# Optimization experiments

Measured on AMD Instinct MI355X. Metric: run time of the kernel, lower is better.

## Reference

```python
import jax, jax.numpy as jnp
import numpy as np

B, S, D, H, L, W, O = 4, 1024, 512, 8, 6, 64, 300
DH = D // H          # head dim = 64
R = 2 * W + 3        # rel_proj output dim = 131
EPS = 1e-6


def setup_inputs() -> dict:
    key = jax.random.key(0)
    ks = jax.random.split(key, 12)
    sc = 0.02
    x = jax.random.normal(ks[0], (B, S, D), jnp.float32)
    inp = {
        "x": x,
        "ln1_g": jnp.ones((L, D), jnp.float32),
        "ln1_b": jnp.zeros((L, D), jnp.float32),
        "qkv_w": jax.random.normal(ks[1], (L, D, 3 * D), jnp.float32) * sc,
        "qkv_b": jnp.zeros((L, 3 * D), jnp.float32),
        "rel_w": jax.random.normal(ks[2], (DH, R), jnp.float32) * sc,
        "rel_b": jnp.zeros((R,), jnp.float32),
        "ln2_g": jnp.ones((L, D), jnp.float32),
        "ln2_b": jnp.zeros((L, D), jnp.float32),
        "mlp_w1": jax.random.normal(ks[3], (L, D, 4 * D), jnp.float32) * sc,
        "mlp_b1": jnp.zeros((L, 4 * D), jnp.float32),
        "mlp_w2": jax.random.normal(ks[4], (L, 4 * D, D), jnp.float32) * sc,
        "mlp_b2": jnp.zeros((L, D), jnp.float32),
        "normf_g": jnp.ones((D,), jnp.float32),
        "normf_b": jnp.zeros((D,), jnp.float32),
        "head_w": jax.random.normal(ks[5], (D, O), jnp.float32) * sc,
        "head_b": jnp.zeros((O,), jnp.float32),
        "mask": jax.random.randint(ks[6], (B, O), 0, 2, jnp.int32),
    }
    return inp


def _layernorm(x, g, b):
    m = jnp.mean(x, axis=-1, keepdims=True)
    v = jnp.mean(jnp.square(x - m), axis=-1, keepdims=True)
    return (x - m) * jax.lax.rsqrt(v + EPS) * g + b


def _forward(x, ln1_g, ln1_b, qkv_w, qkv_b, rel_w, rel_b, ln2_g, ln2_b,
             mlp_w1, mlp_b1, mlp_w2, mlp_b2, normf_g, normf_b, head_w, head_b, mask):
    b, s, d = x.shape
    # clamped relative offsets, shifted to [0, 2W]; shape [s, s]
    ar = jnp.arange(s)
    offsets = jnp.clip(ar[None, :] - ar[:, None], -W, W) + W
    off_bh = jnp.broadcast_to(offsets[None, None], (b, H, s, s))
    scale = 1.0 / np.sqrt(D / H)  # = 1/sqrt(dh)

    def block(xc, lp):
        (l1g, l1b, qw, qb, l2g, l2b, w1, b1, w2, b2) = lp
        h = _layernorm(xc, l1g, l1b)
        qkv = (h @ qw + qb).reshape(b, s, H, 3 * DH)
        q, k, v = jnp.split(qkv, 3, axis=-1)            # [b,s,h,dh] each
        q = q.transpose(0, 2, 1, 3)                     # [b,h,s,dh]
        k = k.transpose(0, 2, 1, 3)
        v = v.transpose(0, 2, 1, 3)
        content = jnp.einsum('bhik,bhjk->bhij', q, k) * scale
        pos = q @ rel_w + rel_b                          # [b,h,s,R]
        pos_scores = jnp.take_along_axis(pos, off_bh, axis=-1)  # [b,h,s,s]
        attn = jax.nn.softmax(content + pos_scores, axis=-1)
        out = jnp.einsum('bhij,bhjk->bhik', attn, v)     # [b,h,s,dh]
        xc = xc + out.transpose(0, 2, 1, 3).reshape(b, s, d)
        h2 = _layernorm(xc, l2g, l2b)
        m = jax.nn.gelu(h2 @ w1 + b1, approximate=False) @ w2 + b2
        return xc + m, None

    layer_params = (ln1_g, ln1_b, qkv_w, qkv_b, ln2_g, ln2_b,
                    mlp_w1, mlp_b1, mlp_w2, mlp_b2)
    x, _ = jax.lax.scan(block, x, layer_params)
    x = _layernorm(x, normf_g, normf_b)[:, 0, :]         # CLS token
    logits = x @ head_w + head_b                          # [b, O]
    return jnp.where(mask == 0, -jnp.inf, logits)


def reference(x, ln1_g, ln1_b, qkv_w, qkv_b, rel_w, rel_b, ln2_g, ln2_b,
              mlp_w1, mlp_b1, mlp_w2, mlp_b2, normf_g, normf_b, head_w, head_b, mask):
    return _forward(x, ln1_g, ln1_b, qkv_w, qkv_b, rel_w, rel_b, ln2_g, ln2_b,
                    mlp_w1, mlp_b1, mlp_w2, mlp_b2, normf_g, normf_b, head_w, head_b, mask)
```

## Files before the change

### kernel.cpp

```cpp
#include <hip/hip_runtime.h>
#include <math.h>

#define B_  4
#define S_  1024
#define D_  512
#define H_  8
#define L_  6
#define W_  64
#define O_  300
#define DH_ 64
#define R_  131
#define R2_ 132

typedef __attribute__((ext_vector_type(8))) short bf16x8;
typedef __attribute__((ext_vector_type(4))) float f32x4;

#define SWZ(r) ((((r) ^ ((r) >> 3)) & 7) << 4)

__device__ __forceinline__ float gelu_f(float x) {
    return 0.5f * x * (1.0f + erff(x * 0.70710678118654752f));
}

__device__ __forceinline__ unsigned short f2bf(float f) {
    union { float f; unsigned u; } c; c.f = f;
    unsigned u = c.u;
    unsigned r = (u + 0x7fffu + ((u >> 16) & 1u)) >> 16;
    return (unsigned short)r;
}
__device__ __forceinline__ float bf2f(unsigned short u) {
    union { unsigned u; float f; } c; c.u = ((unsigned)u) << 16; return c.f;
}

__device__ __forceinline__ void gload_lds16(const void* g, void* l) {
    __builtin_amdgcn_global_load_lds(
        (const __attribute__((address_space(1))) unsigned int*)g,
        (__attribute__((address_space(3))) unsigned int*)l, 16, 0, 0);
}

template<int OB>
__global__ __launch_bounds__(256) void ln_kernel(
    const float* __restrict__ x, const float* __restrict__ g,
    const float* __restrict__ b, void* __restrict__ y,
    int rows, long instride, long outstride)
{
    int wave = threadIdx.x >> 6;
    int lane = threadIdx.x & 63;
    int row  = blockIdx.x * 4 + wave;
    if (row >= rows) return;
    const float* xr = x + (size_t)row * instride;
    float4 v0 = *(const float4*)(xr + lane * 4);
    float4 v1 = *(const float4*)(xr + 256 + lane * 4);

    float s = v0.x + v0.y + v0.z + v0.w + v1.x + v1.y + v1.z + v1.w;
    #pragma unroll
    for (int off = 32; off >= 1; off >>= 1) s += __shfl_xor(s, off);
    float mean = s * (1.0f / 512.0f);

    float a0 = v0.x - mean, a1 = v0.y - mean, a2 = v0.z - mean, a3 = v0.w - mean;
    float a4 = v1.x - mean, a5 = v1.y - mean, a6 = v1.z - mean, a7 = v1.w - mean;
    float vs = a0*a0 + a1*a1 + a2*a2 + a3*a3 + a4*a4 + a5*a5 + a6*a6 + a7*a7;
    #pragma unroll
    for (int off = 32; off >= 1; off >>= 1) vs += __shfl_xor(vs, off);
    float rstd = rsqrtf(vs * (1.0f / 512.0f) + 1e-6f);

    float4 g0 = *(const float4*)(g + lane * 4);
    float4 g1 = *(const float4*)(g + 256 + lane * 4);
    float4 b0 = *(const float4*)(b + lane * 4);
    float4 b1 = *(const float4*)(b + 256 + lane * 4);

    float o0 = a0 * rstd * g0.x + b0.x;
    float o1 = a1 * rstd * g0.y + b0.y;
    float o2 = a2 * rstd * g0.z + b0.z;
    float o3 = a3 * rstd * g0.w + b0.w;
    float o4 = a4 * rstd * g1.x + b1.x;
    float o5 = a5 * rstd * g1.y + b1.y;
    float o6 = a6 * rstd * g1.z + b1.z;
    float o7 = a7 * rstd * g1.w + b1.w;

    if (OB) {
        unsigned short* yr = (unsigned short*)y + (size_t)row * outstride;
        ushort4 p0 = {f2bf(o0), f2bf(o1), f2bf(o2), f2bf(o3)};
        ushort4 p1 = {f2bf(o4), f2bf(o5), f2bf(o6), f2bf(o7)};
        *(ushort4*)(yr + lane * 4)       = p0;
        *(ushort4*)(yr + 256 + lane * 4) = p1;
    } else {
        float* yr = (float*)y + (size_t)row * outstride;
        *(float4*)(yr + lane * 4)       = make_float4(o0, o1, o2, o3);
        *(float4*)(yr + 256 + lane * 4) = make_float4(o4, o5, o6, o7);
    }
}

__global__ __launch_bounds__(256) void tconv_kernel(
    const float* __restrict__ in, unsigned short* __restrict__ out, int K, int N)
{
    __shared__ float t[32][33];
    int tx = threadIdx.x & 31, ty = threadIdx.x >> 5;
    int n0 = blockIdx.x * 32, k0 = blockIdx.y * 32;
    #pragma unroll
    for (int j = 0; j < 4; ++j)
        t[ty + 8*j][tx] = in[(size_t)(k0 + ty + 8*j) * N + n0 + tx];
    __syncthreads();
    #pragma unroll
    for (int j = 0; j < 4; ++j)
        out[(size_t)(n0 + ty + 8*j) * K + k0 + tx] = f2bf(t[tx][ty + 8*j]);
}

__global__ __launch_bounds__(256) void relw_prep(
    const float* __restrict__ rel_w, unsigned short* __restrict__ relwT)
{
    for (int i = threadIdx.x; i < 144 * 64; i += 256) {
        int r = i >> 6, c = i & 63;
        relwT[i] = (r < R_) ? f2bf(rel_w[(size_t)c * R_ + r]) : (unsigned short)0;
    }
}

template<int ACT, int OBF, int BM, int BN, int WM, int WN, int BK>
__global__ __launch_bounds__(256) void mfma_gemm(
    const unsigned short* __restrict__ A, const unsigned short* __restrict__ BT,
    const float* __restrict__ bias, const float* __restrict__ resid,
    void* __restrict__ Cout, int M, int N, int K)
{
    static_assert(WM * WN == 4, "4 waves");
    constexpr int MFR = BM / WM / 16;
    constexpr int NFR = BN / WN / 16;
    constexpr int TPR = BK / 8;
    constexpr int RPP = 256 / TPR;
    __shared__ __align__(16) unsigned short As[BM * BK];
    __shared__ __align__(16) unsigned short Bs[BN * BK];
    int tid  = threadIdx.x;
    int lane = tid & 63;
    int l15 = lane & 15, l4 = lane >> 4;
    int wid  = tid >> 6;
    int wave_m = (wid / WN) * (BM / WM);
    int wave_n = (wid % WN) * (BN / WN);
    int bm = blockIdx.y * BM, bn = blockIdx.x * BN;

    const f32x4 z4 = {0.f, 0.f, 0.f, 0.f};
    f32x4 acc[MFR][NFR];
    #pragma unroll
    for (int m = 0; m < MFR; ++m)
        #pragma unroll
        for (int n = 0; n < NFR; ++n) acc[m][n] = z4;

    int arow = tid / TPR;
    int acol8 = ((tid % TPR) ^ (arow & (TPR - 1))) * 8;
    const unsigned short* Ab = A  + (size_t)(bm + arow) * K + acol8;
    const unsigned short* Bb = BT + (size_t)(bn + arow) * K + acol8;
    unsigned short* Adst = As + tid * 8;
    unsigned short* Bdst = Bs + tid * 8;

    int swzA = l15 & (TPR - 1);
    const unsigned short* Afrag = As + (size_t)(wave_m + l15) * BK;
    const unsigned short* Bfrag = Bs + (size_t)(wave_n + l15) * BK;

    for (int k0 = 0; k0 < K; k0 += BK) {
        #pragma unroll
        for (int ch = 0; ch < BM / RPP; ++ch)
            gload_lds16(Ab + (size_t)ch * RPP * K + k0, Adst + ch * RPP * BK);
        #pragma unroll
        for (int ch = 0; ch < BN / RPP; ++ch)
            gload_lds16(Bb + (size_t)ch * RPP * K + k0, Bdst + ch * RPP * BK);
        __syncthreads();

        #pragma unroll
        for (int kk = 0; kk < BK / 32; ++kk) {
            int off8 = ((l4 + 4 * kk) ^ swzA) * 8;
            bf16x8 af[MFR], bfr[NFR];
            #pragma unroll
            for (int m = 0; m < MFR; ++m) af[m]  = *(const bf16x8*)(Afrag + m * 16 * BK + off8);
            #pragma unroll
            for (int n = 0; n < NFR; ++n) bfr[n] = *(const bf16x8*)(Bfrag + n * 16 * BK + off8);
            #pragma unroll
            for (int m = 0; m < MFR; ++m)
                #pragma unroll
                for (int n = 0; n < NFR; ++n)
                    acc[m][n] = __builtin_amdgcn_mfma_f32_16x16x32_bf16(af[m], bfr[n], acc[m][n], 0, 0, 0);
        }
        __syncthreads();
    }

    int r0 = bm + wave_m + (l4 * 4);
    int c0 = bn + wave_n + l15;
    #pragma unroll
    for (int m = 0; m < MFR; ++m) {
        #pragma unroll
        for (int n = 0; n < NFR; ++n) {
            int c = c0 + n * 16;
            float bv = bias[c];
            #pragma unroll
            for (int q = 0; q < 4; ++q) {
                int r = r0 + m * 16 + q;
                float v = acc[m][n][q] + bv;
                if (ACT == 1) v = gelu_f(v);
                if (resid) v += resid[(size_t)r * N + c];
                if (OBF) ((unsigned short*)Cout)[(size_t)r * N + c] = f2bf(v);
                else     ((float*)Cout)[(size_t)r * N + c] = v;
            }
        }
    }
}

__global__ __launch_bounds__(512, 2) void attn_mfma(
    const unsigned short* __restrict__ qkv,
    const unsigned short* __restrict__ relwT,
    const float* __restrict__ rel_b,
    float* __restrict__ xres)
{
    __shared__ __align__(16) unsigned char shm[66048];
    unsigned char* Klds  = shm;
    unsigned char* Vtlds = shm + 16384;
    unsigned char* Plds  = shm + 32768;
    unsigned short* pos16 = (unsigned short*)(shm + 49152);
    float* mergeO  = (float*)shm;
    float* mergeML = (float*)(shm + 17408);

    int tid = threadIdx.x, lane = tid & 63, w = tid >> 6;
    int l15 = lane & 15, l4 = lane >> 4;
    int wq = w & 3;
    int g  = w >> 2;
    int it0 = blockIdx.x * 64;
    int h = blockIdx.y, b = blockIdx.z;
    const float LOG2E = 1.4426950408889634f;
    const float SC = 0.125f * LOG2E;

    bf16x8 qa[2];
    {
        const unsigned short* qp = qkv + (size_t)(b * S_ + it0 + wq * 16 + l15) * 1536 + h * 192 + l4 * 8;
        qa[0] = *(const bf16x8*)(qp);
        qa[1] = *(const bf16x8*)(qp + 32);
    }

    if (g == 0) {
        #pragma unroll
        for (int n = 0; n < 9; ++n) {
            f32x4 pacc = {0.f, 0.f, 0.f, 0.f};
            #pragma unroll
            for (int ks = 0; ks < 2; ++ks) {
                bf16x8 bv = *(const bf16x8*)(relwT + (size_t)(16 * n + l15) * 64 + ks * 32 + l4 * 8);
                pacc = __builtin_amdgcn_mfma_f32_16x16x32_bf16(qa[ks], bv, pacc, 0, 0, 0);
            }
            int c = 16 * n + l15;
            if (c < R_) {
                float rb = rel_b[c];
                #pragma unroll
                for (int q = 0; q < 4; ++q)
                    pos16[(wq * 16 + l4 * 4 + q) * R2_ + c] = f2bf((pacc[q] + rb) * LOG2E);
            }
        }
    }
    __syncthreads();

    int rloc = wq * 16 + l15;
    int i_glob = it0 + rloc;
    float p_lo = bf2f(pos16[rloc * R2_ + 0]);
    float p_hi = bf2f(pos16[rloc * R2_ + 128]);

    int rf = tid >> 2, seg = tid & 3;
    int gk = rf >> 6, rr = rf & 63;
    const unsigned short* kbase = qkv + (size_t)(b * S_ + gk * 512 + rr) * 1536 + h * 192 + 64 + seg * 16;
    int kbyt = gk * 8192 + ((rr * 128 + seg * 32) ^ SWZ(rr));
    int pf = tid >> 3, seg8 = tid & 7;
    int gv = pf >> 5, pp = pf & 31;
    const unsigned short* vbase = qkv + (size_t)(b * S_ + gv * 512 + 2 * pp) * 1536 + h * 192 + 128 + seg8 * 8;
    bf16x8 kr0, kr1, vr0, vr1;
    kr0 = *(const bf16x8*)(kbase);
    kr1 = *(const bf16x8*)(kbase + 8);
    vr0 = *(const bf16x8*)(vbase);
    vr1 = *(const bf16x8*)(vbase + 1536);

    const f32x4 z4 = {0.f, 0.f, 0.f, 0.f};
    f32x4 oacc[4];
    #pragma unroll
    for (int n = 0; n < 4; ++n) oacc[n] = z4;
    float mrun_s = -INFINITY, lrun_s = 0.f;
    int wmin = it0 + wq * 16;
    unsigned char* Kw = Klds + g * 8192;
    unsigned char* Vw = Vtlds + g * 8192;
    unsigned char* Pw = Plds + w * 2048;

    for (int t = 0; t < 8; ++t) {
        int jt0 = g * 512 + t * 64;
        __syncthreads();
        *(bf16x8*)(Klds + kbyt) = kr0;
        *(bf16x8*)(Klds + (kbyt ^ 16)) = kr1;
        #pragma unroll
        for (int i = 0; i < 8; ++i) {
            int dh = seg8 * 8 + i;
            unsigned v01 = (unsigned)(unsigned short)vr0[i] | ((unsigned)(unsigned short)vr1[i] << 16);
            *(unsigned*)(Vtlds + gv * 8192 + ((dh * 128 + pp * 4) ^ SWZ(dh))) = v01;
        }
        __syncthreads();
        if (t < 7) {
            const unsigned short* kp = kbase + (size_t)(t + 1) * 64 * 1536;
            kr0 = *(const bf16x8*)(kp);
            kr1 = *(const bf16x8*)(kp + 8);
            const unsigned short* vp = vbase + (size_t)(t + 1) * 64 * 1536;
            vr0 = *(const bf16x8*)(vp);
            vr1 = *(const bf16x8*)(vp + 1536);
        }

        f32x4 ssw[4];
        #pragma unroll
        for (int n = 0; n < 4; ++n) ssw[n] = z4;
        #pragma unroll
        for (int n = 0; n < 4; ++n) {
            int kvr = 16 * n + l15;
            #pragma unroll
            for (int ks = 0; ks < 2; ++ks) {
                bf16x8 ak = *(const bf16x8*)(Kw + ((kvr * 128 + ks * 64 + l4 * 16) ^ SWZ(kvr)));
                ssw[n] = __builtin_amdgcn_mfma_f32_16x16x32_bf16(ak, qa[ks], ssw[n], 0, 0, 0);
            }
        }

        float sv[4][4];
        bool left  = (jt0 + 63 < wmin - 64);
        bool right = (jt0 > wmin + 15 + 64);
        if (left || right) {
            float pc = left ? p_lo : p_hi;
            #pragma unroll
            for (int n = 0; n < 4; ++n)
                #pragma unroll
                for (int r = 0; r < 4; ++r) sv[n][r] = fmaf(ssw[n][r], SC, pc);
        } else {
            #pragma unroll
            for (int n = 0; n < 4; ++n)
                #pragma unroll
                for (int r = 0; r < 4; ++r) {
                    int j = jt0 + 16 * n + l4 * 4 + r;
                    int off = j - i_glob;
                    off = off < -64 ? -64 : (off > 64 ? 64 : off);
                    sv[n][r] = fmaf(ssw[n][r], SC, bf2f(pos16[rloc * R2_ + off + 64]));
                }
        }

        float a0 = fmaxf(fmaxf(sv[0][0], sv[0][1]), fmaxf(sv[0][2], sv[0][3]));
        float a1 = fmaxf(fmaxf(sv[1][0], sv[1][1]), fmaxf(sv[1][2], sv[1][3]));
        float a2 = fmaxf(fmaxf(sv[2][0], sv[2][1]), fmaxf(sv[2][2], sv[2][3]));
        float a3 = fmaxf(fmaxf(sv[3][0], sv[3][1]), fmaxf(sv[3][2], sv[3][3]));
        float mx = fmaxf(fmaxf(a0, a1), fmaxf(a2, a3));
        mx = fmaxf(mx, __shfl_xor(mx, 16));
        mx = fmaxf(mx, __shfl_xor(mx, 32));
        float mnew = fmaxf(mrun_s, mx);
        float al = exp2f(mrun_s - mnew);
        mrun_s = mnew;
        float rs = 0.f;
        #pragma unroll
        for (int n = 0; n < 4; ++n)
            #pragma unroll
            for (int r = 0; r < 4; ++r) {
                float p = exp2f(sv[n][r] - mnew);
                sv[n][r] = p;
                rs += p;
            }
        rs += __shfl_xor(rs, 16);
        rs += __shfl_xor(rs, 32);
        lrun_s = lrun_s * al + rs;
        float alv0 = __shfl(al, l4 * 4 + 0);
        float alv1 = __shfl(al, l4 * 4 + 1);
        float alv2 = __shfl(al, l4 * 4 + 2);
        float alv3 = __shfl(al, l4 * 4 + 3);
        #pragma unroll
        for (int n = 0; n < 4; ++n) {
            oacc[n][0] *= alv0; oacc[n][1] *= alv1;
            oacc[n][2] *= alv2; oacc[n][3] *= alv3;
        }

        #pragma unroll
        for (int n = 0; n < 4; ++n) {
            unsigned pk01, pk23;
            asm("v_cvt_pk_bf16_f32 %0, %1, %2" : "=v"(pk01) : "v"(sv[n][0]), "v"(sv[n][1]));
            asm("v_cvt_pk_bf16_f32 %0, %1, %2" : "=v"(pk23) : "v"(sv[n][2]), "v"(sv[n][3]));
            int boff = (l15 * 128 + (16 * n + l4 * 4) * 2) ^ SWZ(l15);
            *(uint2*)(Pw + boff) = make_uint2(pk01, pk23);
        }

        bf16x8 pa[2];
        #pragma unroll
        for (int ks = 0; ks < 2; ++ks)
            pa[ks] = *(const bf16x8*)(Pw + ((l15 * 128 + ks * 64 + l4 * 16) ^ SWZ(l15)));
        #pragma unroll
        for (int n = 0; n < 4; ++n) {
            int dh = 16 * n + l15;
            #pragma unroll
            for (int ks = 0; ks < 2; ++ks) {
                bf16x8 bv = *(const bf16x8*)(Vw + ((dh * 128 + ks * 64 + l4 * 16) ^ SWZ(dh)));
                oacc[n] = __builtin_amdgcn_mfma_f32_16x16x32_bf16(pa[ks], bv, oacc[n], 0, 0, 0);
            }
        }
    }

    __syncthreads();
    if (g == 1) {
        #pragma unroll
        for (int n = 0; n < 4; ++n)
            #pragma unroll
            for (int r = 0; r < 4; ++r)
                mergeO[(wq * 16 + l4 * 4 + r) * 68 + 16 * n + l15] = oacc[n][r];
        if (lane < 16) {
            mergeML[rloc * 2 + 0] = mrun_s;
            mergeML[rloc * 2 + 1] = lrun_s;
        }
    }
    __syncthreads();
    if (g == 0) {
        float mb = mergeML[rloc * 2 + 0];
        float lb = mergeML[rloc * 2 + 1];
        float M  = fmaxf(mrun_s, mb);
        float fa = exp2f(mrun_s - M);
        float fb = exp2f(mb - M);
        float inv = 1.0f / (lrun_s * fa + lb * fb);
        float A_s = fa * inv, B_s = fb * inv;
        float Av[4], Bv[4];
        #pragma unroll
        for (int r = 0; r < 4; ++r) {
            Av[r] = __shfl(A_s, l4 * 4 + r);
            Bv[r] = __shfl(B_s, l4 * 4 + r);
        }
        #pragma unroll
        for (int r = 0; r < 4; ++r) {
            int row = wq * 16 + l4 * 4 + r;
            float* xp = xres + (size_t)(b * S_ + it0 + row) * D_ + h * DH_;
            #pragma unroll
            for (int n = 0; n < 4; ++n)
                xp[16 * n + l15] += oacc[n][r] * Av[r] + mergeO[row * 68 + 16 * n + l15] * Bv[r];
        }
    }
}

__global__ __launch_bounds__(256) void head_kernel(
    const float* __restrict__ hin, const float* __restrict__ hw,
    const float* __restrict__ hbias, const int* __restrict__ mask,
    float* __restrict__ out)
{
    __shared__ float a[4][512];
    __shared__ float part[4][64][4];
    int tid = threadIdx.x;
    #pragma unroll
    for (int i = tid; i < 2048; i += 256) a[i >> 9][i & 511] = hin[i];
    __syncthreads();

    int cl = tid & 63;
    int c  = blockIdx.x * 64 + cl;
    int ks = tid >> 6;
    float ac[4] = {0.f, 0.f, 0.f, 0.f};
    if (c < O_) {
        const float* wp = hw + (size_t)(ks * 128) * O_ + c;
        #pragma unroll 8
        for (int k = 0; k < 128; ++k) {
            float wv = wp[(size_t)k * O_];
            int kk = ks * 128 + k;
            ac[0] = fmaf(a[0][kk], wv, ac[0]);
            ac[1] = fmaf(a[1][kk], wv, ac[1]);
            ac[2] = fmaf(a[2][kk], wv, ac[2]);
            ac[3] = fmaf(a[3][kk], wv, ac[3]);
        }
    }
    #pragma unroll
    for (int bb = 0; bb < 4; ++bb) part[ks][cl][bb] = ac[bb];
    __syncthreads();
    if (ks == 0 && c < O_) {
        float hbv = hbias[c];
        #pragma unroll
        for (int bb = 0; bb < 4; ++bb) {
            float v = part[0][cl][bb] + part[1][cl][bb] + part[2][cl][bb] + part[3][cl][bb] + hbv;
            out[bb * O_ + c] = (mask[bb * O_ + c] == 0) ? -1e30f : v;
        }
    }
}

extern "C" void kernel_launch(void* const* d_in, const int* in_sizes, int n_in,
                              void* d_out, int out_size, void* d_ws, size_t ws_size,
                              hipStream_t stream) {
    const float* x      = (const float*)d_in[0];
    const float* ln1_g  = (const float*)d_in[1];
    const float* ln1_b  = (const float*)d_in[2];
    const float* qkv_w  = (const float*)d_in[3];
    const float* qkv_b  = (const float*)d_in[4];
    const float* rel_w  = (const float*)d_in[5];
    const float* rel_b  = (const float*)d_in[6];
    const float* ln2_g  = (const float*)d_in[7];
    const float* ln2_b  = (const float*)d_in[8];
    const float* mlp_w1 = (const float*)d_in[9];
    const float* mlp_b1 = (const float*)d_in[10];
    const float* mlp_w2 = (const float*)d_in[11];
    const float* mlp_b2 = (const float*)d_in[12];
    const float* normf_g = (const float*)d_in[13];
    const float* normf_b = (const float*)d_in[14];
    const float* head_w  = (const float*)d_in[15];
    const float* head_b  = (const float*)d_in[16];
    const int*   mask    = (const int*)d_in[17];
    float* out = (float*)d_out;
    float* ws  = (float*)d_ws;

    float* x_cur = ws;
    float* reg2  = ws + 2097152;
    float* wregs = ws + 6291456;
    unsigned short* qkv16 = (unsigned short*)reg2;
    unsigned short* midb  = (unsigned short*)reg2;
    unsigned short* hb    = (unsigned short*)wregs;
    unsigned short* wTq   = (unsigned short*)(wregs + 1048576);
    unsigned short* wT1   = (unsigned short*)(wregs + 1441792);
    unsigned short* wT2   = (unsigned short*)(wregs + 1966080);
    unsigned short* relwT = (unsigned short*)(ws + 10616832);
    float* head_in = ws + 10621440;

    const int NR = B_ * S_;
    dim3 blk(256);

    hipMemcpyAsync(x_cur, x, (size_t)NR * D_ * sizeof(float),
                   hipMemcpyDeviceToDevice, stream);
    relw_prep<<<1, blk, 0, stream>>>(rel_w, relwT);

    for (int l = 0; l < L_; ++l) {
        ln_kernel<1><<<NR / 4, blk, 0, stream>>>(x_cur, ln1_g + l * D_, ln1_b + l * D_,
                                                 hb, NR, D_, D_);
        tconv_kernel<<<dim3(48, 16), blk, 0, stream>>>(
            qkv_w + (size_t)l * D_ * 3 * D_, wTq, D_, 3 * D_);
        mfma_gemm<0, 1, 128, 64, 4, 1, 64><<<dim3(24, 32), blk, 0, stream>>>(
            hb, wTq, qkv_b + (size_t)l * 3 * D_, nullptr, qkv16, NR, 3 * D_, D_);
        attn_mfma<<<dim3(S_ / 64, H_, B_), dim3(512), 0, stream>>>(qkv16, relwT, rel_b, x_cur);
        ln_kernel<1><<<NR / 4, blk, 0, stream>>>(x_cur, ln2_g + l * D_, ln2_b + l * D_,
                                                 hb, NR, D_, D_);
        tconv_kernel<<<dim3(64, 16), blk, 0, stream>>>(
            mlp_w1 + (size_t)l * D_ * 4 * D_, wT1, D_, 4 * D_);
        mfma_gemm<1, 1, 128, 64, 4, 1, 64><<<dim3(32, 32), blk, 0, stream>>>(
            hb, wT1, mlp_b1 + (size_t)l * 4 * D_, nullptr, midb, NR, 4 * D_, D_);
        tconv_kernel<<<dim3(16, 64), blk, 0, stream>>>(
            mlp_w2 + (size_t)l * 4 * D_ * D_, wT2, 4 * D_, D_);
        mfma_gemm<0, 0, 64, 64, 2, 2, 64><<<dim3(8, 64), blk, 0, stream>>>(
            midb, wT2, mlp_b2 + (size_t)l * D_, x_cur, x_cur, NR, D_, 4 * D_);
    }

    ln_kernel<0><<<1, blk, 0, stream>>>(x_cur, normf_g, normf_b, head_in,
                                        B_, (long)S_ * D_, D_);
    head_kernel<<<dim3(5), blk, 0, stream>>>(head_in, head_w, head_b, mask, out);
}
```

Before: 706.0 us.

## Batch weight conversion, swizzle GEMM blocks, lazy softmax rescale, fuse final LN

When the workspace is large enough, all layers' weight transposes and bf16 conversions now run in one up-front kernel, replacing three conversion launches per layer. GEMM workgroup ids are remapped in an XCD-aware way to improve L2 locality. The attention online softmax skips rescaling unless the running max grows past a threshold. The final layernorm is fused into the head kernel. Together these cut launch count and per-tile exp and multiply work, at the cost of a larger workspace and a slight numerical risk from the deferred rescale.

```diff
diff --git a/kernel.cpp b/kernel.cpp
--- a/kernel.cpp
+++ b/kernel.cpp
@@ -37,17 +37,15 @@
         (__attribute__((address_space(3))) unsigned int*)l, 16, 0, 0);
 }
 
-template<int OB>
 __global__ __launch_bounds__(256) void ln_kernel(
     const float* __restrict__ x, const float* __restrict__ g,
-    const float* __restrict__ b, void* __restrict__ y,
-    int rows, long instride, long outstride)
+    const float* __restrict__ b, unsigned short* __restrict__ y, int rows)
 {
     int wave = threadIdx.x >> 6;
     int lane = threadIdx.x & 63;
     int row  = blockIdx.x * 4 + wave;
     if (row >= rows) return;
-    const float* xr = x + (size_t)row * instride;
+    const float* xr = x + (size_t)row * D_;
     float4 v0 = *(const float4*)(xr + lane * 4);
     float4 v1 = *(const float4*)(xr + 256 + lane * 4);
 
@@ -68,26 +66,13 @@
     float4 b0 = *(const float4*)(b + lane * 4);
     float4 b1 = *(const float4*)(b + 256 + lane * 4);
 
-    float o0 = a0 * rstd * g0.x + b0.x;
-    float o1 = a1 * rstd * g0.y + b0.y;
-    float o2 = a2 * rstd * g0.z + b0.z;
-    float o3 = a3 * rstd * g0.w + b0.w;
-    float o4 = a4 * rstd * g1.x + b1.x;
-    float o5 = a5 * rstd * g1.y + b1.y;
-    float o6 = a6 * rstd * g1.z + b1.z;
-    float o7 = a7 * rstd * g1.w + b1.w;
-
-    if (OB) {
-        unsigned short* yr = (unsigned short*)y + (size_t)row * outstride;
-        ushort4 p0 = {f2bf(o0), f2bf(o1), f2bf(o2), f2bf(o3)};
-        ushort4 p1 = {f2bf(o4), f2bf(o5), f2bf(o6), f2bf(o7)};
-        *(ushort4*)(yr + lane * 4)       = p0;
-        *(ushort4*)(yr + 256 + lane * 4) = p1;
-    } else {
-        float* yr = (float*)y + (size_t)row * outstride;
-        *(float4*)(yr + lane * 4)       = make_float4(o0, o1, o2, o3);
-        *(float4*)(yr + 256 + lane * 4) = make_float4(o4, o5, o6, o7);
-    }
+    unsigned short* yr = y + (size_t)row * D_;
+    ushort4 p0 = {f2bf(a0 * rstd * g0.x + b0.x), f2bf(a1 * rstd * g0.y + b0.y),
+                  f2bf(a2 * rstd * g0.z + b0.z), f2bf(a3 * rstd * g0.w + b0.w)};
+    ushort4 p1 = {f2bf(a4 * rstd * g1.x + b1.x), f2bf(a5 * rstd * g1.y + b1.y),
+                  f2bf(a6 * rstd * g1.z + b1.z), f2bf(a7 * rstd * g1.w + b1.w)};
+    *(ushort4*)(yr + lane * 4)       = p0;
+    *(ushort4*)(yr + 256 + lane * 4) = p1;
 }
 
 __global__ __launch_bounds__(256) void tconv_kernel(
@@ -112,6 +97,46 @@
         int r = i >> 6, c = i & 63;
         relwT[i] = (r < R_) ? f2bf(rel_w[(size_t)c * R_ + r]) : (unsigned short)0;
     }
+}
+
+__global__ __launch_bounds__(256) void prep_all(
+    const float* __restrict__ qkv_w, const float* __restrict__ mlp_w1,
+    const float* __restrict__ mlp_w2, const float* __restrict__ rel_w,
+    unsigned short* __restrict__ wTq_all, unsigned short* __restrict__ wT1_all,
+    unsigned short* __restrict__ wT2_all, unsigned short* __restrict__ relwT)
+{
+    int bid = blockIdx.x;
+    if (bid >= 16896) {
+        for (int i = threadIdx.x; i < 144 * 64; i += 256) {
+            int r = i >> 6, c = i & 63;
+            relwT[i] = (r < R_) ? f2bf(rel_w[(size_t)c * R_ + r]) : (unsigned short)0;
+        }
+        return;
+    }
+    int l = bid / 2816, rr = bid - l * 2816;
+    const float* in; unsigned short* out; int K, N, bx, by;
+    if (rr < 768) {
+        in = qkv_w + (size_t)l * 512 * 1536; out = wTq_all + (size_t)l * 1536 * 512;
+        K = 512; N = 1536; bx = rr % 48; by = rr / 48;
+    } else if (rr < 1792) {
+        int r2 = rr - 768;
+        in = mlp_w1 + (size_t)l * 512 * 2048; out = wT1_all + (size_t)l * 2048 * 512;
+        K = 512; N = 2048; bx = r2 % 64; by = r2 / 64;
+    } else {
+        int r2 = rr - 1792;
+        in = mlp_w2 + (size_t)l * 2048 * 512; out = wT2_all + (size_t)l * 512 * 2048;
+        K = 2048; N = 512; bx = r2 % 16; by = r2 / 16;
+    }
+    __shared__ float t[32][33];
+    int tx = threadIdx.x & 31, ty = threadIdx.x >> 5;
+    int n0 = bx * 32, k0 = by * 32;
+    #pragma unroll
+    for (int j = 0; j < 4; ++j)
+        t[ty + 8*j][tx] = in[(size_t)(k0 + ty + 8*j) * N + n0 + tx];
+    __syncthreads();
+    #pragma unroll
+    for (int j = 0; j < 4; ++j)
+        out[(size_t)(n0 + ty + 8*j) * K + k0 + tx] = f2bf(t[tx][ty + 8*j]);
 }
 
 template<int ACT, int OBF, int BM, int BN, int WM, int WN, int BK>
@@ -133,7 +158,11 @@
     int wid  = tid >> 6;
     int wave_m = (wid / WN) * (BM / WM);
     int wave_n = (wid % WN) * (BN / WN);
-    int bm = blockIdx.y * BM, bn = blockIdx.x * BN;
+
+    int nwg = gridDim.x * gridDim.y;
+    int bid0 = blockIdx.y * gridDim.x + blockIdx.x;
+    int bid = (bid0 & 7) * (nwg >> 3) + (bid0 >> 3);
+    int bm = (bid / gridDim.x) * BM, bn = (bid % gridDim.x) * BN;
 
     const f32x4 z4 = {0.f, 0.f, 0.f, 0.f};
     f32x4 acc[MFR][NFR];
@@ -222,6 +251,7 @@
     int h = blockIdx.y, b = blockIdx.z;
     const float LOG2E = 1.4426950408889634f;
     const float SC = 0.125f * LOG2E;
+    const float THR = 11.5441f;
 
     bf16x8 qa[2];
     {
@@ -340,30 +370,33 @@
         float mx = fmaxf(fmaxf(a0, a1), fmaxf(a2, a3));
         mx = fmaxf(mx, __shfl_xor(mx, 16));
         mx = fmaxf(mx, __shfl_xor(mx, 32));
-        float mnew = fmaxf(mrun_s, mx);
-        float al = exp2f(mrun_s - mnew);
-        mrun_s = mnew;
+        if (!__all(mx - mrun_s <= THR)) {
+            float mnew = fmaxf(mrun_s, mx);
+            float al = exp2f(mrun_s - mnew);
+            mrun_s = mnew;
+            lrun_s *= al;
+            float alv0 = __shfl(al, l4 * 4 + 0);
+            float alv1 = __shfl(al, l4 * 4 + 1);
+            float alv2 = __shfl(al, l4 * 4 + 2);
+            float alv3 = __shfl(al, l4 * 4 + 3);
+            #pragma unroll
+            for (int n = 0; n < 4; ++n) {
+                oacc[n][0] *= alv0; oacc[n][1] *= alv1;
+                oacc[n][2] *= alv2; oacc[n][3] *= alv3;
+            }
+        }
         float rs = 0.f;
         #pragma unroll
         for (int n = 0; n < 4; ++n)
             #pragma unroll
             for (int r = 0; r < 4; ++r) {
-                float p = exp2f(sv[n][r] - mnew);
+                float p = exp2f(sv[n][r] - mrun_s);
                 sv[n][r] = p;
                 rs += p;
             }
         rs += __shfl_xor(rs, 16);
         rs += __shfl_xor(rs, 32);
-        lrun_s = lrun_s * al + rs;
-        float alv0 = __shfl(al, l4 * 4 + 0);
-        float alv1 = __shfl(al, l4 * 4 + 1);
-        float alv2 = __shfl(al, l4 * 4 + 2);
-        float alv3 = __shfl(al, l4 * 4 + 3);
-        #pragma unroll
-        for (int n = 0; n < 4; ++n) {
-            oacc[n][0] *= alv0; oacc[n][1] *= alv1;
-            oacc[n][2] *= alv2; oacc[n][3] *= alv3;
-        }
+        lrun_s += rs;
 
         #pragma unroll
         for (int n = 0; n < 4; ++n) {
@@ -428,15 +461,42 @@
 }
 
 __global__ __launch_bounds__(256) void head_kernel(
-    const float* __restrict__ hin, const float* __restrict__ hw,
+    const float* __restrict__ xc, const float* __restrict__ gf,
+    const float* __restrict__ bfp, const float* __restrict__ hw,
     const float* __restrict__ hbias, const int* __restrict__ mask,
     float* __restrict__ out)
 {
     __shared__ float a[4][512];
     __shared__ float part[4][64][4];
     int tid = threadIdx.x;
-    #pragma unroll
-    for (int i = tid; i < 2048; i += 256) a[i >> 9][i & 511] = hin[i];
+    int wv = tid >> 6, lane = tid & 63;
+    {
+        const float* xr = xc + (size_t)wv * S_ * D_;
+        float4 v0 = *(const float4*)(xr + lane * 4);
+        float4 v1 = *(const float4*)(xr + 256 + lane * 4);
+        float s = v0.x + v0.y + v0.z + v0.w + v1.x + v1.y + v1.z + v1.w;
+        #pragma unroll
+        for (int off = 32; off >= 1; off >>= 1) s += __shfl_xor(s, off);
+        float mean = s * (1.0f / 512.0f);
+        float c0 = v0.x - mean, c1 = v0.y - mean, c2 = v0.z - mean, c3 = v0.w - mean;
+        float c4 = v1.x - mean, c5 = v1.y - mean, c6 = v1.z - mean, c7 = v1.w - mean;
+        float vs = c0*c0 + c1*c1 + c2*c2 + c3*c3 + c4*c4 + c5*c5 + c6*c6 + c7*c7;
+        #pragma unroll
+        for (int off = 32; off >= 1; off >>= 1) vs += __shfl_xor(vs, off);
+        float rstd = rsqrtf(vs * (1.0f / 512.0f) + 1e-6f);
+        float4 g0 = *(const float4*)(gf + lane * 4);
+        float4 g1 = *(const float4*)(gf + 256 + lane * 4);
+        float4 b0 = *(const float4*)(bfp + lane * 4);
+        float4 b1 = *(const float4*)(bfp + 256 + lane * 4);
+        a[wv][lane * 4 + 0] = c0 * rstd * g0.x + b0.x;
+        a[wv][lane * 4 + 1] = c1 * rstd * g0.y + b0.y;
+        a[wv][lane * 4 + 2] = c2 * rstd * g0.z + b0.z;
+        a[wv][lane * 4 + 3] = c3 * rstd * g0.w + b0.w;
+        a[wv][256 + lane * 4 + 0] = c4 * rstd * g1.x + b1.x;
+        a[wv][256 + lane * 4 + 1] = c5 * rstd * g1.y + b1.y;
+        a[wv][256 + lane * 4 + 2] = c6 * rstd * g1.z + b1.z;
+        a[wv][256 + lane * 4 + 3] = c7 * rstd * g1.w + b1.w;
+    }
     __syncthreads();
 
     int cl = tid & 63;
@@ -447,12 +507,12 @@
         const float* wp = hw + (size_t)(ks * 128) * O_ + c;
         #pragma unroll 8
         for (int k = 0; k < 128; ++k) {
-            float wv = wp[(size_t)k * O_];
+            float wvv = wp[(size_t)k * O_];
             int kk = ks * 128 + k;
-            ac[0] = fmaf(a[0][kk], wv, ac[0]);
-            ac[1] = fmaf(a[1][kk], wv, ac[1]);
-            ac[2] = fmaf(a[2][kk], wv, ac[2]);
-            ac[3] = fmaf(a[3][kk], wv, ac[3]);
+            ac[0] = fmaf(a[0][kk], wvv, ac[0]);
+            ac[1] = fmaf(a[1][kk], wvv, ac[1]);
+            ac[2] = fmaf(a[2][kk], wvv, ac[2]);
+            ac[3] = fmaf(a[3][kk], wvv, ac[3]);
         }
     }
     #pragma unroll
@@ -492,46 +552,72 @@
     float* out = (float*)d_out;
     float* ws  = (float*)d_ws;
 
+    const int NR = B_ * S_;
+    dim3 blk(256);
+
     float* x_cur = ws;
     float* reg2  = ws + 2097152;
-    float* wregs = ws + 6291456;
     unsigned short* qkv16 = (unsigned short*)reg2;
     unsigned short* midb  = (unsigned short*)reg2;
-    unsigned short* hb    = (unsigned short*)wregs;
-    unsigned short* wTq   = (unsigned short*)(wregs + 1048576);
-    unsigned short* wT1   = (unsigned short*)(wregs + 1441792);
-    unsigned short* wT2   = (unsigned short*)(wregs + 1966080);
-    unsigned short* relwT = (unsigned short*)(ws + 10616832);
-    float* head_in = ws + 10621440;
-
-    const int NR = B_ * S_;
-    dim3 blk(256);
 
     hipMemcpyAsync(x_cur, x, (size_t)NR * D_ * sizeof(float),
                    hipMemcpyDeviceToDevice, stream);
-    relw_prep<<<1, blk, 0, stream>>>(rel_w, relwT);
-
-    for (int l = 0; l < L_; ++l) {
-        ln_kernel<1><<<NR / 4, blk, 0, stream>>>(x_cur, ln1_g + l * D_, ln1_b + l * D_,
-                                                 hb, NR, D_, D_);
-        tconv_kernel<<<dim3(48, 16), blk, 0, stream>>>(
-            qkv_w + (size_t)l * D_ * 3 * D_, wTq, D_, 3 * D_);
-        mfma_gemm<0, 1, 128, 64, 4, 1, 64><<<dim3(24, 32), blk, 0, stream>>>(
-            hb, wTq, qkv_b + (size_t)l * 3 * D_, nullptr, qkv16, NR, 3 * D_, D_);
-        attn_mfma<<<dim3(S_ / 64, H_, B_), dim3(512), 0, stream>>>(qkv16, relwT, rel_b, x_cur);
-        ln_kernel<1><<<NR / 4, blk, 0, stream>>>(x_cur, ln2_g + l * D_, ln2_b + l * D_,
-                                                 hb, NR, D_, D_);
-        tconv_kernel<<<dim3(64, 16), blk, 0, stream>>>(
-            mlp_w1 + (size_t)l * D_ * 4 * D_, wT1, D_, 4 * D_);
-        mfma_gemm<1, 1, 128, 64, 4, 1, 64><<<dim3(32, 32), blk, 0, stream>>>(
-            hb, wT1, mlp_b1 + (size_t)l * 4 * D_, nullptr, midb, NR, 4 * D_, D_);
-        tconv_kernel<<<dim3(16, 64), blk, 0, stream>>>(
-            mlp_w2 + (size_t)l * 4 * D_ * D_, wT2, 4 * D_, D_);
-        mfma_gemm<0, 0, 64, 64, 2, 2, 64><<<dim3(8, 64), blk, 0, stream>>>(
-            midb, wT2, mlp_b2 + (size_t)l * D_, x_cur, x_cur, NR, D_, 4 * D_);
-    }
-
-    ln_kernel<0><<<1, blk, 0, stream>>>(x_cur, normf_g, normf_b, head_in,
-                                        B_, (long)S_ * D_, D_);
-    head_kernel<<<dim3(5), blk, 0, stream>>>(head_in, head_w, head_b, mask, out);
-}
+
+    bool hoist = ws_size >= (size_t)15995392 * 4;
+
+    if (hoist) {
+        unsigned short* hb      = (unsigned short*)(ws + 6291456);
+        unsigned short* wTq_all = (unsigned short*)(ws + 7340032);
+        unsigned short* wT1_all = (unsigned short*)(ws + 9699328);
+        unsigned short* wT2_all = (unsigned short*)(ws + 12845056);
+        unsigned short* relwT   = (unsigned short*)(ws + 15990784);
+
+        prep_all<<<16897, blk, 0, stream>>>(qkv_w, mlp_w1, mlp_w2, rel_w,
+                                            wTq_all, wT1_all, wT2_all, relwT);
+
+        for (int l = 0; l < L_; ++l) {
+            ln_kernel<<<NR / 4, blk, 0, stream>>>(x_cur, ln1_g + l * D_, ln1_b + l * D_, hb, NR);
+            mfma_gemm<0, 1, 128, 64, 4, 1, 64><<<dim3(24, 32), blk, 0, stream>>>(
+                hb, wTq_all + (size_t)l * 1536 * 512, qkv_b + (size_t)l * 3 * D_,
+                nullptr, qkv16, NR, 3 * D_, D_);
+            attn_mfma<<<dim3(S_ / 64, H_, B_), dim3(512), 0, stream>>>(qkv16, relwT, rel_b, x_cur);
+            ln_kernel<<<NR / 4, blk, 0, stream>>>(x_cur, ln2_g + l * D_, ln2_b + l * D_, hb, NR);
+            mfma_gemm<1, 1, 128, 64, 4, 1, 64><<<dim3(32, 32), blk, 0, stream>>>(
+                hb, wT1_all + (size_t)l * 2048 * 512, mlp_b1 + (size_t)l * 4 * D_,
+                nullptr, midb, NR, 4 * D_, D_);
+            mfma_gemm<0, 0, 64, 64, 2, 2, 64><<<dim3(8, 64), blk, 0, stream>>>(
+                midb, wT2_all + (size_t)l * 512 * 2048, mlp_b2 + (size_t)l * D_,
+                x_cur, x_cur, NR, D_, 4 * D_);
+        }
+        head_kernel<<<dim3(5), blk, 0, stream>>>(x_cur, normf_g, normf_b,
+                                                 head_w, head_b, mask, out);
+    } else {
+        float* wregs = ws + 6291456;
+        unsigned short* hb    = (unsigned short*)wregs;
+        unsigned short* wTq   = (unsigned short*)(wregs + 1048576);
+        unsigned short* wT1   = (unsigned short*)(wregs + 1441792);
+        unsigned short* wT2   = (unsigned short*)(wregs + 1966080);
+        unsigned short* relwT = (unsigned short*)(ws + 10616832);
+
+        relw_prep<<<1, blk, 0, stream>>>(rel_w, relwT);
+        for (int l = 0; l < L_; ++l) {
+            ln_kernel<<<NR / 4, blk, 0, stream>>>(x_cur, ln1_g + l * D_, ln1_b + l * D_, hb, NR);
+            tconv_kernel<<<dim3(48, 16), blk, 0, stream>>>(
+                qkv_w + (size_t)l * D_ * 3 * D_, wTq, D_, 3 * D_);
+            mfma_gemm<0, 1, 128, 64, 4, 1, 64><<<dim3(24, 32), blk, 0, stream>>>(
+                hb, wTq, qkv_b + (size_t)l * 3 * D_, nullptr, qkv16, NR, 3 * D_, D_);
+            attn_mfma<<<dim3(S_ / 64, H_, B_), dim3(512), 0, stream>>>(qkv16, relwT, rel_b, x_cur);
+            ln_kernel<<<NR / 4, blk, 0, stream>>>(x_cur, ln2_g + l * D_, ln2_b + l * D_, hb, NR);
+            tconv_kernel<<<dim3(64, 16), blk, 0, stream>>>(
+                mlp_w1 + (size_t)l * D_ * 4 * D_, wT1, D_, 4 * D_);
+            mfma_gemm<1, 1, 128, 64, 4, 1, 64><<<dim3(32, 32), blk, 0, stream>>>(
+                hb, wT1, mlp_b1 + (size_t)l * 4 * D_, nullptr, midb, NR, 4 * D_, D_);
+            tconv_kernel<<<dim3(16, 64), blk, 0, stream>>>(
+                mlp_w2 + (size_t)l * 4 * D_ * D_, wT2, 4 * D_, D_);
+            mfma_gemm<0, 0, 64, 64, 2, 2, 64><<<dim3(8, 64), blk, 0, stream>>>(
+                midb, wT2, mlp_b2 + (size_t)l * D_, x_cur, x_cur, NR, D_, 4 * D_);
+        }
+        head_kernel<<<dim3(5), blk, 0, stream>>>(x_cur, normf_g, normf_b,
+                                                 head_w, head_b, mask, out);
+    }
+}
```

Result: faster. 650.5 us (-7.9%).
